# Kernel tuning notes

Hardware: AMD Instinct MI355X
Metric: run time of the kernel (lower is better)

The kernel has to match this reference:

```python
import jax, jax.numpy as jnp
import numpy as np

B, X, Y, T = 8, 256, 256, 64   # input grid; T == fno_width
MODES = 16
PAD = 8
T_LOOKBACK = 16
SCALE = 1.0 / (T * T_LOOKBACK)  # 1/(fno_width*t_lookback)


def setup_inputs() -> dict:
    key = jax.random.key(0)
    ks = jax.random.split(key, 5)
    m = MODES
    x = jax.random.normal(ks[0], (B, X, Y, T), dtype=jnp.float32)
    w_tl = SCALE * jax.random.uniform(ks[1], (m, m, m), dtype=jnp.float32)
    w_tr = SCALE * jax.random.uniform(ks[2], (m, m, m), dtype=jnp.float32)
    w_bl = SCALE * jax.random.uniform(ks[3], (m, m, m), dtype=jnp.float32)
    w_br = SCALE * jax.random.uniform(ks[4], (m, m, m), dtype=jnp.float32)
    z = jnp.zeros((m, m, m), dtype=jnp.float32)
    return {"x": x, "w_tl": w_tl, "w_tr": w_tr, "w_bl": w_bl, "w_br": w_br,
            "b_tl": z, "b_tr": z, "b_bl": z, "b_br": z}


def reference(x, w_tl, w_tr, w_bl, w_br, b_tl, b_tr, b_bl, b_br):
    m, pad = MODES, PAD
    # pad all three non-batch dims
    xp = jnp.pad(x, ((0, 0), (pad, pad), (pad, pad), (pad, pad)))
    # tf: x = complex(x, x); x_ft = real(fft3d(x)) == Re(F(a)) - Im(F(a))
    xc = jax.lax.complex(xp, xp)
    x_ft = jnp.real(jnp.fft.fftn(xc, axes=(1, 2, 3)))
    # four corner mode blocks along axes 1,2; low modes along axis 3
    m_tl = x_ft[:, :m, :m, :m]
    m_tr = x_ft[:, -m:, :m, :m]
    m_bl = x_ft[:, :m, -m:, :m]
    m_br = x_ft[:, -m:, -m:, :m]
    top = jnp.concatenate([m_tl * w_tl + b_tl, m_tr * w_tr + b_tr], axis=1)
    bot = jnp.concatenate([m_bl * w_bl + b_bl, m_br * w_br + b_br], axis=1)
    xwb = jnp.concatenate([top, bot], axis=2)  # [B, 2m, 2m, m]
    # pad back to the UNPADDED input shape (axes 1,2) and to fno_width (axis 3)
    xwb = jnp.pad(xwb, ((0, 0), (0, X - 2 * m), (0, Y - 2 * m), (0, T - m)))
    # tf: output = real(ifft3d(complex(xwb, xwb)))
    out = jnp.real(jnp.fft.ifftn(jax.lax.complex(xwb, xwb), axes=(1, 2, 3)))
    return out
```

## Files before the change

kernel.cpp:

```cpp
#include <hip/hip_runtime.h>

#define PI_D 3.141592653589793238462643383279502884


__global__ void k_tables(float2* __restrict__ wt, float2* __restrict__ wxy,
                         float2* __restrict__ vt, float2* __restrict__ vxy,
                         float2* __restrict__ pqf, float2* __restrict__ pqi) {
  int t = blockIdx.x * blockDim.x + threadIdx.x;
  if (t < 64 * 16) {
    int n3 = t >> 4, k3 = t & 15;
    int ph = (k3 * (n3 + 8)) % 80;
    double a = -2.0 * PI_D * (double)ph / 80.0;
    wt[t] = make_float2((float)cos(a), (float)sin(a));
  }
  if (t < 256 * 32) {
    int n = t >> 5, k = t & 31;
    int kk = (k < 16) ? k : (240 + k);
    int ph = (kk * (n + 8)) % 272;
    double a = -2.0 * PI_D * (double)ph / 272.0;
    double c = cos(a), s = sin(a);
    wxy[t] = make_float2((float)c, (float)s);
    pqf[t] = make_float2((float)(c - s), (float)(-(c + s)));
  }
  if (t < 16 * 64) {
    int k3 = t >> 6, n3 = t & 63;
    int ph = (k3 * n3) & 63;
    double a = 2.0 * PI_D * (double)ph / 64.0;
    vt[t] = make_float2((float)cos(a), (float)sin(a));
  }
  if (t < 256 * 32) {
    int n = t >> 5, k = t & 31;
    int ph = (k * n) & 255;
    double a = 2.0 * PI_D * (double)ph / 256.0;
    double c = cos(a), s = sin(a);
    vxy[t] = make_float2((float)c, (float)s);
    const double inv = 1.0 / 4194304.0;
    pqi[t] = make_float2((float)((c - s) * inv), (float)((-(c + s)) * inv));
  }
}

__global__ __launch_bounds__(256) void k_fft_t(const float* __restrict__ x,
                                               float2* __restrict__ A,
                                               const float2* __restrict__ wt) {
  __shared__ float sX[64][65];
  __shared__ float2 swt[1024];
  long blk = blockIdx.x;
  int tid = threadIdx.x;
  const float4* xg = (const float4*)(x + blk * 4096);
#pragma unroll
  for (int e = 0; e < 4; e++) {
    int idx = tid + e * 256;
    float4 v = xg[idx];
    int r = idx >> 4, c = (idx & 15) * 4;
    sX[r][c] = v.x; sX[r][c + 1] = v.y; sX[r][c + 2] = v.z; sX[r][c + 3] = v.w;
  }
#pragma unroll
  for (int e = 0; e < 4; e++) swt[tid + e * 256] = wt[tid + e * 256];
  __syncthreads();
  int r = tid >> 2, q = (tid & 3) * 4;
  float2 a0 = {0,0}, a1 = {0,0}, a2 = {0,0}, a3 = {0,0};
#pragma unroll 8
  for (int n3 = 0; n3 < 64; n3++) {
    float xv = sX[r][n3];
    const float2* wr = &swt[n3 * 16 + q];
    float2 w0 = wr[0], w1 = wr[1], w2 = wr[2], w3 = wr[3];
    a0.x = fmaf(xv, w0.x, a0.x); a0.y = fmaf(xv, w0.y, a0.y);
    a1.x = fmaf(xv, w1.x, a1.x); a1.y = fmaf(xv, w1.y, a1.y);
    a2.x = fmaf(xv, w2.x, a2.x); a2.y = fmaf(xv, w2.y, a2.y);
    a3.x = fmaf(xv, w3.x, a3.x); a3.y = fmaf(xv, w3.y, a3.y);
  }
  float4* Ao = (float4*)(A + (blk * 64 + r) * 16 + q);
  Ao[0] = make_float4(a0.x, a0.y, a1.x, a1.y);
  Ao[1] = make_float4(a2.x, a2.y, a3.x, a3.y);
}

__global__ __launch_bounds__(256) void k_fft_y(const float2* __restrict__ A,
                                               float2* __restrict__ Bm,
                                               const float2* __restrict__ wxy) {
  __shared__ float2 sA[4096];
  __shared__ float2 sW[2048];
  int bn1 = blockIdx.x;
  int tid = threadIdx.x;
  const float4* Ag = (const float4*)(A + (long)bn1 * 4096);
  float4* sA4 = (float4*)sA;
#pragma unroll
  for (int e = 0; e < 8; e++) sA4[tid + e * 256] = Ag[tid + e * 256];
  int k2 = tid >> 3, p = (tid & 7) * 2;
  float2 r0 = {0,0}, r1 = {0,0};
  const float4* wg4 = (const float4*)wxy;
  float4* sW4 = (float4*)sW;
  for (int ch = 0; ch < 4; ch++) {
    __syncthreads();
#pragma unroll
    for (int e = 0; e < 4; e++) sW4[tid + e * 256] = wg4[ch * 1024 + tid + e * 256];
    __syncthreads();
#pragma unroll 4
    for (int t = 0; t < 64; t++) {
      float4 av = *(const float4*)&sA[(ch * 64 + t) * 16 + p];
      float2 w = sW[t * 32 + k2];
      r0.x = fmaf(av.x, w.x, r0.x); r0.x = fmaf(-av.y, w.y, r0.x);
      r0.y = fmaf(av.x, w.y, r0.y); r0.y = fmaf(av.y, w.x, r0.y);
      r1.x = fmaf(av.z, w.x, r1.x); r1.x = fmaf(-av.w, w.y, r1.x);
      r1.y = fmaf(av.z, w.y, r1.y); r1.y = fmaf(av.w, w.x, r1.y);
    }
  }
  float4* Bo = (float4*)(Bm + (long)bn1 * 512 + k2 * 16 + p);
  *Bo = make_float4(r0.x, r0.y, r1.x, r1.y);
}

__global__ __launch_bounds__(512) void k_fft_x(
    const float2* __restrict__ Bm, float* __restrict__ y,
    const float2* __restrict__ pqf,
    const float* __restrict__ w_tl, const float* __restrict__ w_tr,
    const float* __restrict__ w_bl, const float* __restrict__ w_br,
    const float* __restrict__ b_tl, const float* __restrict__ b_tr,
    const float* __restrict__ b_bl, const float* __restrict__ b_br) {
  __shared__ float2 sB[4096];
  __shared__ float2 sPQ[8192];
  int b = blockIdx.x >> 5, k2 = blockIdx.x & 31;
  int tid = threadIdx.x;
  for (int i = tid; i < 4096; i += 512) {
    sB[i] = Bm[((long)(b * 256 + (i >> 4)) * 32 + k2) * 16 + (i & 15)];
  }
  const float4* pq4 = (const float4*)pqf;
  float4* sPQ4 = (float4*)sPQ;
#pragma unroll
  for (int e = 0; e < 8; e++) sPQ4[tid + e * 512] = pq4[tid + e * 512];
  __syncthreads();
  int k1 = tid >> 4, k3 = tid & 15;
  float acc = 0.f;
#pragma unroll 8
  for (int n1 = 0; n1 < 256; n1++) {
    float2 a = sB[n1 * 16 + k3];
    float2 w = sPQ[n1 * 32 + k1];
    acc = fmaf(a.x, w.x, acc);
    acc = fmaf(a.y, w.y, acc);
  }
  const float* wsel = (k1 < 16) ? ((k2 < 16) ? w_tl : w_bl) : ((k2 < 16) ? w_tr : w_br);
  const float* bsel = (k1 < 16) ? ((k2 < 16) ? b_tl : b_bl) : ((k2 < 16) ? b_tr : b_br);
  int idx = ((k1 & 15) * 16 + (k2 & 15)) * 16 + k3;
  y[((b * 32 + k1) * 32 + k2) * 16 + k3] = fmaf(acc, wsel[idx], bsel[idx]);
}

__global__ __launch_bounds__(256) void k_inv_te(const float* __restrict__ y,
                                                float2* __restrict__ E,
                                                const float2* __restrict__ vt,
                                                const float2* __restrict__ vxy) {
  __shared__ float sy[512];
  __shared__ float2 svt[1024];
  __shared__ float sD[32][132];
  __shared__ float sV[128][66];
  int blk = blockIdx.x;
  int h = blk & 1, bk1 = blk >> 1;
  int tid = threadIdx.x;
  ((float2*)sy)[tid] = ((const float2*)(y + (long)bk1 * 512))[tid];
#pragma unroll
  for (int e = 0; e < 4; e++) svt[tid + e * 256] = vt[tid + e * 256];
#pragma unroll
  for (int e = 0; e < 16; e++) {
    int q = tid + e * 256;
    int n2l = q >> 5, k2 = q & 31;
    float2 v = vxy[(h * 128 + n2l) * 32 + k2];
    *(float2*)&sV[n2l][2 * k2] = v;
  }
  __syncthreads();
#pragma unroll
  for (int e = 0; e < 8; e++) {
    int idx = tid + e * 256;
    int k2 = idx >> 6, n3i = idx & 63;
    float ax = 0.f, ay = 0.f;
#pragma unroll
    for (int k3 = 0; k3 < 16; k3++) {
      float yv = sy[k2 * 16 + k3];
      float2 v = svt[k3 * 64 + n3i];
      ax = fmaf(yv, v.x, ax); ay = fmaf(yv, v.y, ay);
    }
    *(float2*)&sD[k2][2 * n3i] = make_float2(ax, ay);
  }
  __syncthreads();
  int rg = tid >> 3, tn = tid & 7;
  float acc[4][16];
#pragma unroll
  for (int i = 0; i < 4; i++)
#pragma unroll
    for (int j = 0; j < 16; j++) acc[i][j] = 0.f;
#pragma unroll 2
  for (int k2 = 0; k2 < 32; k2++) {
    float4 d0 = *(const float4*)&sD[k2][tn * 16];
    float4 d1 = *(const float4*)&sD[k2][tn * 16 + 4];
    float4 d2 = *(const float4*)&sD[k2][tn * 16 + 8];
    float4 d3 = *(const float4*)&sD[k2][tn * 16 + 12];
#pragma unroll
    for (int i = 0; i < 4; i++) {
      float2 v = *(const float2*)&sV[rg * 4 + i][2 * k2];
      float c = v.x, s = v.y;
      acc[i][0]  = fmaf(c, d0.x, fmaf(-s, d0.y, acc[i][0]));
      acc[i][1]  = fmaf(c, d0.y, fmaf( s, d0.x, acc[i][1]));
      acc[i][2]  = fmaf(c, d0.z, fmaf(-s, d0.w, acc[i][2]));
      acc[i][3]  = fmaf(c, d0.w, fmaf( s, d0.z, acc[i][3]));
      acc[i][4]  = fmaf(c, d1.x, fmaf(-s, d1.y, acc[i][4]));
      acc[i][5]  = fmaf(c, d1.y, fmaf( s, d1.x, acc[i][5]));
      acc[i][6]  = fmaf(c, d1.z, fmaf(-s, d1.w, acc[i][6]));
      acc[i][7]  = fmaf(c, d1.w, fmaf( s, d1.z, acc[i][7]));
      acc[i][8]  = fmaf(c, d2.x, fmaf(-s, d2.y, acc[i][8]));
      acc[i][9]  = fmaf(c, d2.y, fmaf( s, d2.x, acc[i][9]));
      acc[i][10] = fmaf(c, d2.z, fmaf(-s, d2.w, acc[i][10]));
      acc[i][11] = fmaf(c, d2.w, fmaf( s, d2.z, acc[i][11]));
      acc[i][12] = fmaf(c, d3.x, fmaf(-s, d3.y, acc[i][12]));
      acc[i][13] = fmaf(c, d3.y, fmaf( s, d3.x, acc[i][13]));
      acc[i][14] = fmaf(c, d3.z, fmaf(-s, d3.w, acc[i][14]));
      acc[i][15] = fmaf(c, d3.w, fmaf( s, d3.z, acc[i][15]));
    }
  }
#pragma unroll
  for (int i = 0; i < 4; i++) {
    int n2g = h * 128 + rg * 4 + i;
    float4* dst = (float4*)&E[((long)bk1 * 256 + n2g) * 64 + tn * 8];
    dst[0] = make_float4(acc[i][0], acc[i][1], acc[i][2], acc[i][3]);
    dst[1] = make_float4(acc[i][4], acc[i][5], acc[i][6], acc[i][7]);
    dst[2] = make_float4(acc[i][8], acc[i][9], acc[i][10], acc[i][11]);
    dst[3] = make_float4(acc[i][12], acc[i][13], acc[i][14], acc[i][15]);
  }
}

__global__ __launch_bounds__(256) void k_ifft_x(const float2* __restrict__ E,
                                                float* __restrict__ out,
                                                const float2* __restrict__ pqi) {
  __shared__ float sW[64][256];
  __shared__ float sD[64][64];
  int blk = blockIdx.x;
  int tc = blk & 255, b = blk >> 8;
  int tid = threadIdx.x;
  {
    const float4* pq4 = (const float4*)pqi;
#pragma unroll
    for (int r = 0; r < 16; r++) {
      float4 v = pq4[tid * 16 + r];
      sW[4 * r][tid] = v.x; sW[4 * r + 1][tid] = v.y;
      sW[4 * r + 2][tid] = v.z; sW[4 * r + 3][tid] = v.w;
    }
  }
  {
    const float4* Eg = (const float4*)E;
#pragma unroll
    for (int e = 0; e < 2; e++) {
      int tq = tid + e * 256;
      int k1 = tq >> 4, cq = tq & 15;
      const float4* src = Eg + ((long)(b * 32 + k1) * 8192) + tc * 32 + 2 * cq;
      float4 v0 = src[0], v1 = src[1];
      *(float4*)&sD[2 * k1][4 * cq]     = make_float4(v0.x, v0.z, v1.x, v1.z);
      *(float4*)&sD[2 * k1 + 1][4 * cq] = make_float4(v0.y, v0.w, v1.y, v1.w);
    }
  }
  __syncthreads();
  int tm = tid >> 3, tn = tid & 7;
  float acc[8][8];
#pragma unroll
  for (int i = 0; i < 8; i++)
#pragma unroll
    for (int j = 0; j < 8; j++) acc[i][j] = 0.f;
#pragma unroll 2
  for (int kk = 0; kk < 64; kk++) {
    float4 wa = *(const float4*)&sW[kk][tm * 8];
    float4 wb = *(const float4*)&sW[kk][tm * 8 + 4];
    float4 da = *(const float4*)&sD[kk][tn * 8];
    float4 db = *(const float4*)&sD[kk][tn * 8 + 4];
    float w[8] = {wa.x, wa.y, wa.z, wa.w, wb.x, wb.y, wb.z, wb.w};
    float d[8] = {da.x, da.y, da.z, da.w, db.x, db.y, db.z, db.w};
#pragma unroll
    for (int i = 0; i < 8; i++)
#pragma unroll
      for (int j = 0; j < 8; j++) acc[i][j] = fmaf(w[i], d[j], acc[i][j]);
  }
  float* ob = out + (long)b * 4194304 + (long)(tm * 8) * 16384 + tc * 64 + tn * 8;
#pragma unroll
  for (int i = 0; i < 8; i++) {
    float4* o = (float4*)(ob + (long)i * 16384);
    o[0] = make_float4(acc[i][0], acc[i][1], acc[i][2], acc[i][3]);
    o[1] = make_float4(acc[i][4], acc[i][5], acc[i][6], acc[i][7]);
  }
}

extern "C" void kernel_launch(void* const* d_in, const int* in_sizes, int n_in,
                              void* d_out, int out_size, void* d_ws, size_t ws_size,
                              hipStream_t stream) {
  const float* x    = (const float*)d_in[0];
  const float* w_tl = (const float*)d_in[1];
  const float* w_tr = (const float*)d_in[2];
  const float* w_bl = (const float*)d_in[3];
  const float* w_br = (const float*)d_in[4];
  const float* b_tl = (const float*)d_in[5];
  const float* b_tr = (const float*)d_in[6];
  const float* b_bl = (const float*)d_in[7];
  const float* b_br = (const float*)d_in[8];
  float* out = (float*)d_out;
  char* ws = (char*)d_ws;

  float2* Bm  = (float2*)(ws + 0);
  float*  y   = (float*)(ws + 8388608);
  float2* E   = (float2*)(ws + 10485760);
  float2* WT  = (float2*)(ws + 44040192);
  float2* WXY = (float2*)(ws + 44048384);
  float2* VT  = (float2*)(ws + 44113920);
  float2* VXY = (float2*)(ws + 44122112);
  float2* PQF = (float2*)(ws + 44187648);
  float2* PQI = (float2*)(ws + 44253184);
  float2* A = (float2*)d_out;

  k_tables<<<32, 256, 0, stream>>>(WT, WXY, VT, VXY, PQF, PQI);
  k_fft_t<<<8192, 256, 0, stream>>>(x, A, WT);
  k_fft_y<<<2048, 256, 0, stream>>>(A, Bm, WXY);
  k_fft_x<<<256, 512, 0, stream>>>(Bm, y, PQF, w_tl, w_tr, w_bl, w_br,
                                   b_tl, b_tr, b_bl, b_br);
  k_inv_te<<<512, 256, 0, stream>>>(y, E, VT, VXY);
  k_ifft_x<<<2048, 256, 0, stream>>>(E, out, PQI);
}
```

Baseline: 216.1 us.

## Fuse T-axis and Y-axis forward DFT stages into one kernel

Merges the separate T-axis DFT kernel and the Y-axis DFT kernel into a single kernel that processes one (b,n1) slab of 256x64 inputs per block. The intermediate A tensor now stays in shared memory instead of being written to and re-read from global memory. The large Y twiddle table is replaced by two small factor tables whose product gives each twiddle in registers. Each block now does more work with a swizzled shared-memory layout, and the Y reduction is split across half-waves and combined with a shuffle. This adds register pressure and extra multiplies per step, and the grid is much smaller.

```diff
diff --git a/kernel.cpp b/kernel.cpp
--- a/kernel.cpp
+++ b/kernel.cpp
@@ -3,9 +3,10 @@
 #define PI_D 3.141592653589793238462643383279502884
 
 
-__global__ void k_tables(float2* __restrict__ wt, float2* __restrict__ wxy,
-                         float2* __restrict__ vt, float2* __restrict__ vxy,
-                         float2* __restrict__ pqf, float2* __restrict__ pqi) {
+__global__ void k_tables(float2* __restrict__ wt, float2* __restrict__ vt,
+                         float2* __restrict__ vxy,
+                         float2* __restrict__ pqf, float2* __restrict__ pqi,
+                         float2* __restrict__ t16, float2* __restrict__ t1) {
   int t = blockIdx.x * blockDim.x + threadIdx.x;
   if (t < 64 * 16) {
     int n3 = t >> 4, k3 = t & 15;
@@ -19,8 +20,17 @@
     int ph = (kk * (n + 8)) % 272;
     double a = -2.0 * PI_D * (double)ph / 272.0;
     double c = cos(a), s = sin(a);
-    wxy[t] = make_float2((float)c, (float)s);
     pqf[t] = make_float2((float)(c - s), (float)(-(c + s)));
+  }
+  if (t < 512) {
+    int a = t >> 5, k = t & 31;
+    int kk = (k < 16) ? k : (240 + k);
+    int ph16 = (kk * 16 * a) % 272;
+    double a16 = -2.0 * PI_D * (double)ph16 / 272.0;
+    t16[t] = make_float2((float)cos(a16), (float)sin(a16));
+    int ph1 = (kk * (a + 8)) % 272;
+    double a1 = -2.0 * PI_D * (double)ph1 / 272.0;
+    t1[t] = make_float2((float)cos(a1), (float)sin(a1));
   }
   if (t < 16 * 64) {
     int k3 = t >> 6, n3 = t & 63;
@@ -39,73 +49,90 @@
   }
 }
 
-__global__ __launch_bounds__(256) void k_fft_t(const float* __restrict__ x,
-                                               float2* __restrict__ A,
-                                               const float2* __restrict__ wt) {
-  __shared__ float sX[64][65];
-  __shared__ float2 swt[1024];
-  long blk = blockIdx.x;
-  int tid = threadIdx.x;
-  const float4* xg = (const float4*)(x + blk * 4096);
-#pragma unroll
-  for (int e = 0; e < 4; e++) {
-    int idx = tid + e * 256;
-    float4 v = xg[idx];
-    int r = idx >> 4, c = (idx & 15) * 4;
-    sX[r][c] = v.x; sX[r][c + 1] = v.y; sX[r][c + 2] = v.z; sX[r][c + 3] = v.w;
-  }
-#pragma unroll
-  for (int e = 0; e < 4; e++) swt[tid + e * 256] = wt[tid + e * 256];
-  __syncthreads();
-  int r = tid >> 2, q = (tid & 3) * 4;
-  float2 a0 = {0,0}, a1 = {0,0}, a2 = {0,0}, a3 = {0,0};
-#pragma unroll 8
-  for (int n3 = 0; n3 < 64; n3++) {
-    float xv = sX[r][n3];
-    const float2* wr = &swt[n3 * 16 + q];
-    float2 w0 = wr[0], w1 = wr[1], w2 = wr[2], w3 = wr[3];
-    a0.x = fmaf(xv, w0.x, a0.x); a0.y = fmaf(xv, w0.y, a0.y);
-    a1.x = fmaf(xv, w1.x, a1.x); a1.y = fmaf(xv, w1.y, a1.y);
-    a2.x = fmaf(xv, w2.x, a2.x); a2.y = fmaf(xv, w2.y, a2.y);
-    a3.x = fmaf(xv, w3.x, a3.x); a3.y = fmaf(xv, w3.y, a3.y);
-  }
-  float4* Ao = (float4*)(A + (blk * 64 + r) * 16 + q);
-  Ao[0] = make_float4(a0.x, a0.y, a1.x, a1.y);
-  Ao[1] = make_float4(a2.x, a2.y, a3.x, a3.y);
-}
-
-__global__ __launch_bounds__(256) void k_fft_y(const float2* __restrict__ A,
-                                               float2* __restrict__ Bm,
-                                               const float2* __restrict__ wxy) {
-  __shared__ float2 sA[4096];
-  __shared__ float2 sW[2048];
+__global__ __launch_bounds__(512) void k_fwd(const float* __restrict__ x,
+                                             float2* __restrict__ Bm,
+                                             const float* __restrict__ wtf,
+                                             const float2* __restrict__ t16,
+                                             const float2* __restrict__ t1) {
+  __shared__ float sX[64][260];
+  __shared__ float sAt[256][36];
   int bn1 = blockIdx.x;
   int tid = threadIdx.x;
-  const float4* Ag = (const float4*)(A + (long)bn1 * 4096);
-  float4* sA4 = (float4*)sA;
-#pragma unroll
-  for (int e = 0; e < 8; e++) sA4[tid + e * 256] = Ag[tid + e * 256];
-  int k2 = tid >> 3, p = (tid & 7) * 2;
-  float2 r0 = {0,0}, r1 = {0,0};
-  const float4* wg4 = (const float4*)wxy;
-  float4* sW4 = (float4*)sW;
-  for (int ch = 0; ch < 4; ch++) {
-    __syncthreads();
-#pragma unroll
-    for (int e = 0; e < 4; e++) sW4[tid + e * 256] = wg4[ch * 1024 + tid + e * 256];
-    __syncthreads();
+  int lane = tid & 63;
+  int wv = __builtin_amdgcn_readfirstlane(tid >> 6);
+  const float4* xg = (const float4*)(x + (long)bn1 * 16384);
+#pragma unroll
+  for (int e = 0; e < 8; e++) {
+    int g = tid + e * 512;
+    int n2 = g >> 4, q3 = g & 15;
+    float4 v = xg[g];
+    int cs = n2 ^ ((q3 & 7) * 4);
+    sX[4 * q3 + 0][cs] = v.x; sX[4 * q3 + 1][cs] = v.y;
+    sX[4 * q3 + 2][cs] = v.z; sX[4 * q3 + 3][cs] = v.w;
+  }
+  __syncthreads();
+  {
+    int q = wv & 3, hf = wv >> 2;
+    int n2a = hf * 128 + 2 * lane;
+    float2 acc[2][4];
+#pragma unroll
+    for (int i = 0; i < 2; i++)
+#pragma unroll
+      for (int k = 0; k < 4; k++) acc[i][k] = make_float2(0.f, 0.f);
+    const float* wrow = wtf + 8 * q;
 #pragma unroll 4
-    for (int t = 0; t < 64; t++) {
-      float4 av = *(const float4*)&sA[(ch * 64 + t) * 16 + p];
-      float2 w = sW[t * 32 + k2];
-      r0.x = fmaf(av.x, w.x, r0.x); r0.x = fmaf(-av.y, w.y, r0.x);
-      r0.y = fmaf(av.x, w.y, r0.y); r0.y = fmaf(av.y, w.x, r0.y);
-      r1.x = fmaf(av.z, w.x, r1.x); r1.x = fmaf(-av.w, w.y, r1.x);
-      r1.y = fmaf(av.z, w.y, r1.y); r1.y = fmaf(av.w, w.x, r1.y);
-    }
-  }
-  float4* Bo = (float4*)(Bm + (long)bn1 * 512 + k2 * 16 + p);
-  *Bo = make_float4(r0.x, r0.y, r1.x, r1.y);
+    for (int n3 = 0; n3 < 64; n3++) {
+      float2 xv = *(const float2*)&sX[n3][n2a ^ (((n3 >> 2) & 7) * 4)];
+      float4 wA = *(const float4*)(wrow + n3 * 32);
+      float4 wB = *(const float4*)(wrow + n3 * 32 + 4);
+      acc[0][0].x = fmaf(xv.x, wA.x, acc[0][0].x); acc[0][0].y = fmaf(xv.x, wA.y, acc[0][0].y);
+      acc[0][1].x = fmaf(xv.x, wA.z, acc[0][1].x); acc[0][1].y = fmaf(xv.x, wA.w, acc[0][1].y);
+      acc[0][2].x = fmaf(xv.x, wB.x, acc[0][2].x); acc[0][2].y = fmaf(xv.x, wB.y, acc[0][2].y);
+      acc[0][3].x = fmaf(xv.x, wB.z, acc[0][3].x); acc[0][3].y = fmaf(xv.x, wB.w, acc[0][3].y);
+      acc[1][0].x = fmaf(xv.y, wA.x, acc[1][0].x); acc[1][0].y = fmaf(xv.y, wA.y, acc[1][0].y);
+      acc[1][1].x = fmaf(xv.y, wA.z, acc[1][1].x); acc[1][1].y = fmaf(xv.y, wA.w, acc[1][1].y);
+      acc[1][2].x = fmaf(xv.y, wB.x, acc[1][2].x); acc[1][2].y = fmaf(xv.y, wB.y, acc[1][2].y);
+      acc[1][3].x = fmaf(xv.y, wB.z, acc[1][3].x); acc[1][3].y = fmaf(xv.y, wB.w, acc[1][3].y);
+    }
+#pragma unroll
+    for (int i = 0; i < 2; i++) {
+      int row = n2a + i;
+      *(float4*)&sAt[row][8 * q] =
+          make_float4(acc[i][0].x, acc[i][0].y, acc[i][1].x, acc[i][1].y);
+      *(float4*)&sAt[row][8 * q + 4] =
+          make_float4(acc[i][2].x, acc[i][2].y, acc[i][3].x, acc[i][3].y);
+    }
+  }
+  int k2 = lane & 31, s = lane >> 5;
+  float2 W16[16], W1[16];
+#pragma unroll
+  for (int a = 0; a < 16; a++) {
+    W16[a] = t16[a * 32 + k2];
+    W1[a]  = t1[a * 32 + k2];
+  }
+  __syncthreads();
+  {
+    int p = wv;
+    float2 a0 = make_float2(0.f, 0.f), a1 = make_float2(0.f, 0.f);
+#pragma unroll 8
+    for (int t = 0; t < 128; t++) {
+      int n2 = 2 * t + s;
+      float4 av = *(const float4*)&sAt[n2][4 * p];
+      float2 wa = W16[n2 >> 4], wb = W1[n2 & 15];
+      float wx = fmaf(wa.x, wb.x, -wa.y * wb.y);
+      float wy = fmaf(wa.x, wb.y, wa.y * wb.x);
+      a0.x = fmaf(av.x, wx, fmaf(-av.y, wy, a0.x));
+      a0.y = fmaf(av.x, wy, fmaf(av.y, wx, a0.y));
+      a1.x = fmaf(av.z, wx, fmaf(-av.w, wy, a1.x));
+      a1.y = fmaf(av.z, wy, fmaf(av.w, wx, a1.y));
+    }
+    a0.x += __shfl_xor(a0.x, 32); a0.y += __shfl_xor(a0.y, 32);
+    a1.x += __shfl_xor(a1.x, 32); a1.y += __shfl_xor(a1.y, 32);
+    if (s == 0) {
+      *(float4*)&Bm[(long)bn1 * 512 + k2 * 16 + 2 * p] =
+          make_float4(a0.x, a0.y, a1.x, a1.y);
+    }
+  }
 }
 
 __global__ __launch_bounds__(512) void k_fft_x(
@@ -300,16 +327,15 @@
   float*  y   = (float*)(ws + 8388608);
   float2* E   = (float2*)(ws + 10485760);
   float2* WT  = (float2*)(ws + 44040192);
-  float2* WXY = (float2*)(ws + 44048384);
-  float2* VT  = (float2*)(ws + 44113920);
-  float2* VXY = (float2*)(ws + 44122112);
-  float2* PQF = (float2*)(ws + 44187648);
-  float2* PQI = (float2*)(ws + 44253184);
-  float2* A = (float2*)d_out;
-
-  k_tables<<<32, 256, 0, stream>>>(WT, WXY, VT, VXY, PQF, PQI);
-  k_fft_t<<<8192, 256, 0, stream>>>(x, A, WT);
-  k_fft_y<<<2048, 256, 0, stream>>>(A, Bm, WXY);
+  float2* VT  = (float2*)(ws + 44048384);
+  float2* VXY = (float2*)(ws + 44056576);
+  float2* PQF = (float2*)(ws + 44122112);
+  float2* PQI = (float2*)(ws + 44187648);
+  float2* T16 = (float2*)(ws + 44253184);
+  float2* T1  = (float2*)(ws + 44257280);
+
+  k_tables<<<32, 256, 0, stream>>>(WT, VT, VXY, PQF, PQI, T16, T1);
+  k_fwd<<<2048, 512, 0, stream>>>(x, Bm, (const float*)WT, T16, T1);
   k_fft_x<<<256, 512, 0, stream>>>(Bm, y, PQF, w_tl, w_tr, w_bl, w_br,
                                    b_tl, b_tr, b_bl, b_br);
   k_inv_te<<<512, 256, 0, stream>>>(y, E, VT, VXY);
```

After: 262.4 us. +21.4%, slower.
